# Optimization experiments

Hardware: AMD Instinct MI355X
Metric: run time of the kernel (lower is better)

## Reference

```python
import jax, jax.numpy as jnp
import numpy as np
import math

D_MODEL = 1024
N_HEADS = 16
D_K = D_MODEL // N_HEADS
THETA = 0.1


def setup_inputs() -> dict:
    key = jax.random.key(0)
    ks = jax.random.split(key, 6)
    scale = np.sqrt(1.0 / D_MODEL).astype(np.float32)
    x = jax.random.normal(ks[0], (4, 2048, D_MODEL), dtype=jnp.float32)
    W_q = jax.random.normal(ks[1], (D_MODEL, D_MODEL), dtype=jnp.float32) * scale
    W_k = jax.random.normal(ks[2], (D_MODEL, D_MODEL), dtype=jnp.float32) * scale
    W_v = jax.random.normal(ks[3], (D_MODEL, D_MODEL), dtype=jnp.float32) * scale
    W_o = jax.random.normal(ks[4], (D_MODEL, D_MODEL), dtype=jnp.float32) * scale
    alpha = jnp.ones((1,), dtype=jnp.float32)
    return {"x": x, "W_q": W_q, "W_k": W_k, "W_v": W_v, "W_o": W_o, "alpha": alpha}


def reference(x, W_q, W_k, W_v, W_o, alpha):
    B, S, _ = x.shape
    Q = x @ W_q
    K = x @ W_k
    V = x @ W_v
    # non-commutative elementwise transforms
    Q = Q + THETA * jnp.sin(Q)
    K = K + THETA * jnp.cos(K)
    V = V + alpha * THETA * jnp.tanh(V)
    # split heads: [B, H, S, d_k]
    def split(t):
        return t.reshape(B, S, N_HEADS, D_K).transpose(0, 2, 1, 3)
    Qh, Kh, Vh = split(Q), split(K), split(V)
    scores = jnp.einsum('bhqd,bhkd->bhqk', Qh, Kh) / math.sqrt(D_K)
    attn = jax.nn.softmax(scores, axis=-1)
    out = jnp.einsum('bhqk,bhkd->bhqd', attn, Vh)
    out = out.transpose(0, 2, 1, 3).reshape(B, S, D_MODEL)
    return out @ W_o
```

## Files before the change

### kernel.cpp

```cpp
#include <hip/hip_runtime.h>

typedef __bf16 bf16x8 __attribute__((ext_vector_type(8)));
typedef float f32x4 __attribute__((ext_vector_type(4)));
typedef float f32x16 __attribute__((ext_vector_type(16)));

#define MFMA16(a,b,c) __builtin_amdgcn_mfma_f32_16x16x32_bf16(a,b,c,0,0,0)
#define MFMA32(a,b,c) __builtin_amdgcn_mfma_f32_32x32x16_bf16(a,b,c,0,0,0)

__device__ __forceinline__ unsigned short f2bf(float f) {
  unsigned int u = __float_as_uint(f);
  u = (u + 0x7FFFu + ((u >> 16) & 1u)) >> 16;
  return (unsigned short)u;
}

__device__ __forceinline__ void gload16(const void* g, void* l) {
  __builtin_amdgcn_global_load_lds(
      (const __attribute__((address_space(1))) void*)g,
      (__attribute__((address_space(3))) void*)l, 16, 0, 0);
}

__device__ __forceinline__ float vexp2(float x) {
  float r;
  asm("v_exp_f32 %0, %1" : "=v"(r) : "v"(x));
  return r;
}

__device__ __forceinline__ bf16x8 mk_pfrag(int hi, float p0, float p1, float p2, float p3,
                                           float p4, float p5, float p6, float p7) {
  unsigned int a0, a1, b0, b1;
  asm("v_cvt_pk_bf16_f32 %0, %1, %2" : "=v"(a0) : "v"(p0), "v"(p1));
  asm("v_cvt_pk_bf16_f32 %0, %1, %2" : "=v"(a1) : "v"(p2), "v"(p3));
  asm("v_cvt_pk_bf16_f32 %0, %1, %2" : "=v"(b0) : "v"(p4), "v"(p5));
  asm("v_cvt_pk_bf16_f32 %0, %1, %2" : "=v"(b1) : "v"(p6), "v"(p7));
  unsigned int x = __shfl_xor(hi ? a0 : b0, 32);
  unsigned int y = __shfl_xor(hi ? a1 : b1, 32);
  uint4 w;
  w.x = hi ? x : a0;
  w.y = hi ? y : a1;
  w.z = hi ? b0 : x;
  w.w = hi ? b1 : y;
  return *reinterpret_cast<bf16x8*>(&w);
}

__global__ __launch_bounds__(256) void k_convx(const float* __restrict__ x,
                                               unsigned short* __restrict__ xb) {
  int i = (blockIdx.x * 256 + threadIdx.x) * 4;
  float4 v = *reinterpret_cast<const float4*>(x + i);
  ushort4 o;
  o.x = f2bf(v.x); o.y = f2bf(v.y); o.z = f2bf(v.z); o.w = f2bf(v.w);
  *reinterpret_cast<ushort4*>(xb + i) = o;
}

__global__ __launch_bounds__(256) void k_transw(const float* __restrict__ W,
                                                unsigned short* __restrict__ WT) {
  __shared__ float t[32][33];
  int bx = blockIdx.x * 32;
  int by = blockIdx.y * 32;
  int tx = threadIdx.x & 31;
  int ty = threadIdx.x >> 5;
#pragma unroll
  for (int i = 0; i < 32; i += 8)
    t[ty + i][tx] = W[(size_t)(by + ty + i) * 1024 + bx + tx];
  __syncthreads();
#pragma unroll
  for (int i = 0; i < 32; i += 8)
    WT[(size_t)(bx + ty + i) * 1024 + by + tx] = f2bf(t[tx][ty + i]);
}

template <int EPI>
__global__ __launch_bounds__(256) void k_gemm(
    const unsigned short* __restrict__ A, const unsigned short* __restrict__ BT, int K,
    unsigned short* __restrict__ Qf, unsigned short* __restrict__ Kf,
    unsigned short* __restrict__ VT, const float* __restrict__ alphaPtr,
    float* __restrict__ Out) {
  __shared__ __align__(16) unsigned short smem[128 * 136];
  unsigned short* As = smem;
  unsigned short* Bs = smem + 8192;
  const int tid = threadIdx.x;
  const int wave = tid >> 6, lane = tid & 63;
  const int l15 = lane & 15, lg = lane >> 4;
  const int l7 = l15 & 7;
  const int wr = wave >> 1, wc = wave & 1;
  const int bm = blockIdx.x, bn = blockIdx.y;

  f32x4 acc[4][4] = {};
  const unsigned short* Ab = A + (size_t)bm * 128 * K;
  const unsigned short* Bb = BT + (size_t)bn * 128 * K;

  const int srow = wave * 8 + (lane >> 3);
  const int scol = ((lane & 7) ^ (lane >> 3)) << 3;

  for (int k0 = 0; k0 < K; k0 += 64) {
#pragma unroll
    for (int c = 0; c < 4; ++c) {
      gload16((const void*)(Ab + (size_t)(32 * c + srow) * K + k0 + scol),
              (char*)As + c * 4096 + wave * 1024);
      gload16((const void*)(Bb + (size_t)(32 * c + srow) * K + k0 + scol),
              (char*)Bs + c * 4096 + wave * 1024);
    }
    __syncthreads();
#pragma unroll
    for (int kk = 0; kk < 2; ++kk) {
      bf16x8 af[4], bfr[4];
#pragma unroll
      for (int mi = 0; mi < 4; ++mi) {
        int R = wr * 64 + mi * 16 + l15;
        af[mi] = *reinterpret_cast<const bf16x8*>(&As[R * 64 + (((kk * 4 + lg)) ^ l7) * 8]);
      }
#pragma unroll
      for (int ni = 0; ni < 4; ++ni) {
        int R = wc * 64 + ni * 16 + l15;
        bfr[ni] = *reinterpret_cast<const bf16x8*>(&Bs[R * 64 + (((kk * 4 + lg)) ^ l7) * 8]);
      }
      __builtin_amdgcn_s_setprio(1);
#pragma unroll
      for (int mi = 0; mi < 4; ++mi)
#pragma unroll
        for (int ni = 0; ni < 4; ++ni)
          acc[mi][ni] = MFMA16(af[mi], bfr[ni], acc[mi][ni]);
      __builtin_amdgcn_s_setprio(0);
    }
    __syncthreads();
  }

  if (EPI == 0) {
    const float av = alphaPtr[0];
    const int t = bn >> 3;
    if (t == 2) {
#pragma unroll
      for (int mi = 0; mi < 4; ++mi) {
        int row0 = bm * 128 + wr * 64 + mi * 16 + lg * 4;
        int bb = row0 >> 11, s = row0 & 2047;
#pragma unroll
        for (int ni = 0; ni < 4; ++ni) {
          int col = (bn & 7) * 128 + wc * 64 + ni * 16 + l15;
          int hh = col >> 6, dd = col & 63;
          ushort4 pk;
#pragma unroll
          for (int r = 0; r < 4; ++r) {
            float v = acc[mi][ni][r];
            float e = __expf(2.0f * v);
            v += av * 0.1f * (1.0f - 2.0f * __builtin_amdgcn_rcpf(e + 1.0f));
            ((unsigned short*)&pk)[r] = f2bf(v);
          }
          *reinterpret_cast<ushort4*>(VT + ((size_t)(bb * 16 + hh) * 64 + dd) * 2048 + s) = pk;
        }
      }
    } else {
#pragma unroll
      for (int mi = 0; mi < 4; ++mi)
#pragma unroll
        for (int ni = 0; ni < 4; ++ni)
#pragma unroll
          for (int r = 0; r < 4; ++r) {
            int row = wr * 64 + mi * 16 + lg * 4 + r;
            int col = wc * 64 + ni * 16 + l15;
            float v = acc[mi][ni][r];
            if (t == 0) {
              v += 0.1f * __sinf(v);
              v *= 0.18033688011112042f;
            } else {
              v += 0.1f * __cosf(v);
            }
            smem[row * 136 + col] = f2bf(v);
          }
      __syncthreads();
      unsigned short* dst = (t == 0) ? Qf : Kf;
      const int c16 = tid & 15, rb = tid >> 4;
      const int ncol0 = (bn & 7) * 128;
#pragma unroll
      for (int i2 = 0; i2 < 8; ++i2) {
        int srow2 = rb + i2 * 16;
        uint4 val = *reinterpret_cast<const uint4*>(&smem[srow2 * 136 + c16 * 8]);
        *reinterpret_cast<uint4*>(dst + (size_t)(bm * 128 + srow2) * 1024 + ncol0 + c16 * 8) = val;
      }
    }
  } else {
#pragma unroll
    for (int ni = 0; ni < 4; ++ni) {
      int n = bn * 128 + wc * 64 + ni * 16 + l15;
#pragma unroll
      for (int mi = 0; mi < 4; ++mi) {
        int row = bm * 128 + wr * 64 + mi * 16 + lg * 4;
#pragma unroll
        for (int r = 0; r < 4; ++r)
          Out[(size_t)(row + r) * 1024 + n] = acc[mi][ni][r];
      }
    }
  }
}

__global__ __launch_bounds__(256)
__attribute__((amdgpu_waves_per_eu(4, 4)))
void k_attn(const unsigned short* __restrict__ Qf,
            const unsigned short* __restrict__ Kf,
            const unsigned short* __restrict__ VT,
            unsigned short* __restrict__ AO) {
  __shared__ __align__(16) unsigned short smem[3 * 8192];
  const int tid = threadIdx.x;
  const int wave = tid >> 6, lane = tid & 63;
  const int l31 = lane & 31, hi = lane >> 5;
  const int f = (blockIdx.y << 4) | blockIdx.x;
  const int nf = ((f & 7) << 7) | (f >> 3);
  const int qb = nf & 15, bh = nf >> 4;
  const int b = bh >> 4, h = bh & 15;

  const unsigned short* Qb = Qf + ((size_t)b * 2048 + qb * 128 + wave * 32) * 1024 + h * 64;
  const unsigned short* Kb = Kf + (size_t)b * 2048 * 1024 + h * 64;
  const unsigned short* Vb = VT + (size_t)bh * 64 * 2048;

  bf16x8 qfr[4];
#pragma unroll
  for (int ds = 0; ds < 4; ++ds)
    qfr[ds] = *reinterpret_cast<const bf16x8*>(Qb + (size_t)l31 * 1024 + ds * 16 + hi * 8);
  asm volatile("s_waitcnt vmcnt(0)" ::: "memory");

  float lsum = 0.f;
  f32x16 o0 = {}, o1 = {};

  const int krow0 = wave * 16 + (lane >> 3);
  const int ksrcc = ((lane & 7) ^ (lane >> 3)) << 3;
  const int kxor = l31 & 7;

#pragma unroll
  for (int tt = 0; tt < 2; ++tt) {
    char* Kd = (char*)(smem + tt * 8192) + wave * 2048;
    char* Vd = (char*)(smem + tt * 8192 + 4096) + wave * 2048;
    int kn = tt * 64;
    gload16((const void*)(Kb + (size_t)(kn + krow0) * 1024 + ksrcc), Kd);
    gload16((const void*)(Kb + (size_t)(kn + krow0 + 8) * 1024 + ksrcc), Kd + 1024);
    gload16((const void*)(Vb + (size_t)krow0 * 2048 + kn + ksrcc), Vd);
    gload16((const void*)(Vb + (size_t)(krow0 + 8) * 2048 + kn + ksrcc), Vd + 1024);
  }

  for (int t = 0; t < 32; ++t) {
    const unsigned short* KsC = smem + (t % 3) * 8192;
    const unsigned short* VTC = KsC + 4096;

    if (t < 31) asm volatile("s_waitcnt vmcnt(4)" ::: "memory");
    else        asm volatile("s_waitcnt vmcnt(0)" ::: "memory");
    __builtin_amdgcn_s_barrier();
    __builtin_amdgcn_sched_barrier(0);

    if (t < 30) {
      int kn = (t + 2) * 64;
      char* Kd = (char*)(smem + ((t + 2) % 3) * 8192) + wave * 2048;
      char* Vd = (char*)(smem + ((t + 2) % 3) * 8192 + 4096) + wave * 2048;
      gload16((const void*)(Kb + (size_t)(kn + krow0) * 1024 + ksrcc), Kd);
      gload16((const void*)(Kb + (size_t)(kn + krow0 + 8) * 1024 + ksrcc), Kd + 1024);
      gload16((const void*)(Vb + (size_t)krow0 * 2048 + kn + ksrcc), Vd);
      gload16((const void*)(Vb + (size_t)(krow0 + 8) * 2048 + kn + ksrcc), Vd + 1024);
    }

    f32x16 s0 = {}, s1 = {};
    __builtin_amdgcn_s_setprio(1);
#pragma unroll
    for (int ds = 0; ds < 4; ++ds) {
      int ch = ((ds * 2 + hi) ^ kxor) * 8;
      bf16x8 kf0 = *reinterpret_cast<const bf16x8*>(&KsC[l31 * 64 + ch]);
      bf16x8 kf1 = *reinterpret_cast<const bf16x8*>(&KsC[(l31 + 32) * 64 + ch]);
      s0 = MFMA32(kf0, qfr[ds], s0);
      s1 = MFMA32(kf1, qfr[ds], s1);
    }
    __builtin_amdgcn_s_setprio(0);

    float rs0 = 0.f, rs1 = 0.f, rs2 = 0.f, rs3 = 0.f;
#pragma unroll
    for (int r = 0; r < 16; r += 4) {
      float p0 = vexp2(s0[r]);     s0[r] = p0;     rs0 += p0;
      float p1 = vexp2(s0[r + 1]); s0[r + 1] = p1; rs1 += p1;
      float p2 = vexp2(s0[r + 2]); s0[r + 2] = p2; rs2 += p2;
      float p3 = vexp2(s0[r + 3]); s0[r + 3] = p3; rs3 += p3;
    }
#pragma unroll
    for (int r = 0; r < 16; r += 4) {
      float p0 = vexp2(s1[r]);     s1[r] = p0;     rs0 += p0;
      float p1 = vexp2(s1[r + 1]); s1[r + 1] = p1; rs1 += p1;
      float p2 = vexp2(s1[r + 2]); s1[r + 2] = p2; rs2 += p2;
      float p3 = vexp2(s1[r + 3]); s1[r + 3] = p3; rs3 += p3;
    }
    lsum += (rs0 + rs1) + (rs2 + rs3);

    __builtin_amdgcn_s_setprio(1);
#pragma unroll
    for (int ks = 0; ks < 4; ++ks) {
      bf16x8 pf =
          (ks == 0) ? mk_pfrag(hi, s0[0], s0[1], s0[2], s0[3], s0[4], s0[5], s0[6], s0[7])
        : (ks == 1) ? mk_pfrag(hi, s0[8], s0[9], s0[10], s0[11], s0[12], s0[13], s0[14], s0[15])
        : (ks == 2) ? mk_pfrag(hi, s1[0], s1[1], s1[2], s1[3], s1[4], s1[5], s1[6], s1[7])
                    : mk_pfrag(hi, s1[8], s1[9], s1[10], s1[11], s1[12], s1[13], s1[14], s1[15]);
      int ch = ((ks * 2 + hi) ^ kxor) * 8;
      bf16x8 v0 = *reinterpret_cast<const bf16x8*>(&VTC[l31 * 64 + ch]);
      bf16x8 v1 = *reinterpret_cast<const bf16x8*>(&VTC[(l31 + 32) * 64 + ch]);
      o0 = MFMA32(v0, pf, o0);
      o1 = MFMA32(v1, pf, o1);
    }
    __builtin_amdgcn_s_setprio(0);
  }
  __syncthreads();

  lsum += __shfl_xor(lsum, 32);
  const float inv = 1.0f / lsum;
  unsigned short* OL = smem + wave * 2304;
#pragma unroll
  for (int r = 0; r < 16; ++r) {
    int d0 = (r & 3) + 8 * (r >> 2) + 4 * hi;
    OL[l31 * 72 + d0] = f2bf(o0[r] * inv);
    OL[l31 * 72 + 32 + d0] = f2bf(o1[r] * inv);
  }
  __syncthreads();
#pragma unroll
  for (int p = 0; p < 4; ++p) {
    int u = tid + p * 256;
    int row = u >> 3, ch = u & 7;
    uint4 val = *reinterpret_cast<const uint4*>(&smem[(row >> 5) * 2304 + (row & 31) * 72 + ch * 8]);
    *reinterpret_cast<uint4*>(AO + ((size_t)b * 2048 + qb * 128 + row) * 1024 + h * 64 + ch * 8) = val;
  }
}

extern "C" void kernel_launch(void* const* d_in, const int* in_sizes, int n_in,
                              void* d_out, int out_size, void* d_ws, size_t ws_size,
                              hipStream_t stream) {
  const float* x = (const float*)d_in[0];
  const float* Wq = (const float*)d_in[1];
  const float* Wk = (const float*)d_in[2];
  const float* Wv = (const float*)d_in[3];
  const float* Wo = (const float*)d_in[4];
  const float* alpha = (const float*)d_in[5];
  float* out = (float*)d_out;

  char* ws = (char*)d_ws;
  unsigned short* xb  = (unsigned short*)(ws);
  unsigned short* WT3 = (unsigned short*)(ws + 16777216);
  unsigned short* WoT = (unsigned short*)(ws + 23068672);
  unsigned short* Qf  = (unsigned short*)(ws + 25165824);
  unsigned short* Kf  = (unsigned short*)(ws + 41943040);
  unsigned short* VTb = (unsigned short*)(ws + 58720256);
  unsigned short* AO  = (unsigned short*)(ws + 75497472);

  k_convx<<<dim3(8192), dim3(256), 0, stream>>>(x, xb);
  k_transw<<<dim3(32, 32), dim3(256), 0, stream>>>(Wq, WT3);
  k_transw<<<dim3(32, 32), dim3(256), 0, stream>>>(Wk, WT3 + 1024 * 1024);
  k_transw<<<dim3(32, 32), dim3(256), 0, stream>>>(Wv, WT3 + 2 * 1024 * 1024);
  k_transw<<<dim3(32, 32), dim3(256), 0, stream>>>(Wo, WoT);

  k_gemm<0><<<dim3(64, 24), dim3(256), 0, stream>>>(xb, WT3, 1024, Qf, Kf, VTb, alpha, nullptr);
  k_attn<<<dim3(16, 64), dim3(256), 0, stream>>>(Qf, Kf, VTb, AO);
  k_gemm<1><<<dim3(64, 8), dim3(256), 0, stream>>>(AO, WoT, 1024, nullptr, nullptr, nullptr, nullptr, out);
}
```

Before: 219.4 us.

## Process two 128-row query tiles per attention block to reuse K/V tiles

```diff
diff --git a/kernel.cpp b/kernel.cpp
--- a/kernel.cpp
+++ b/kernel.cpp
@@ -191,7 +191,6 @@
 }
 
 __global__ __launch_bounds__(256)
-__attribute__((amdgpu_waves_per_eu(4, 4)))
 void k_attn(const unsigned short* __restrict__ Qf,
             const unsigned short* __restrict__ Kf,
             const unsigned short* __restrict__ VT,
@@ -200,23 +199,26 @@
   const int tid = threadIdx.x;
   const int wave = tid >> 6, lane = tid & 63;
   const int l31 = lane & 31, hi = lane >> 5;
-  const int f = (blockIdx.y << 4) | blockIdx.x;
-  const int nf = ((f & 7) << 7) | (f >> 3);
-  const int qb = nf & 15, bh = nf >> 4;
+  const int f = (blockIdx.y << 3) | blockIdx.x;
+  const int nf = ((f & 7) << 6) | (f >> 3);
+  const int qb = nf & 7, bh = nf >> 3;
   const int b = bh >> 4, h = bh & 15;
 
-  const unsigned short* Qb = Qf + ((size_t)b * 2048 + qb * 128 + wave * 32) * 1024 + h * 64;
+  const unsigned short* QbA = Qf + ((size_t)b * 2048 + qb * 256 + wave * 32) * 1024 + h * 64;
+  const unsigned short* QbB = QbA + (size_t)128 * 1024;
   const unsigned short* Kb = Kf + (size_t)b * 2048 * 1024 + h * 64;
   const unsigned short* Vb = VT + (size_t)bh * 64 * 2048;
 
-  bf16x8 qfr[4];
-#pragma unroll
-  for (int ds = 0; ds < 4; ++ds)
-    qfr[ds] = *reinterpret_cast<const bf16x8*>(Qb + (size_t)l31 * 1024 + ds * 16 + hi * 8);
+  bf16x8 qfrA[4], qfrB[4];
+#pragma unroll
+  for (int ds = 0; ds < 4; ++ds) {
+    qfrA[ds] = *reinterpret_cast<const bf16x8*>(QbA + (size_t)l31 * 1024 + ds * 16 + hi * 8);
+    qfrB[ds] = *reinterpret_cast<const bf16x8*>(QbB + (size_t)l31 * 1024 + ds * 16 + hi * 8);
+  }
   asm volatile("s_waitcnt vmcnt(0)" ::: "memory");
 
-  float lsum = 0.f;
-  f32x16 o0 = {}, o1 = {};
+  float lsumA = 0.f, lsumB = 0.f;
+  f32x16 o0a = {}, o1a = {}, o0b = {}, o1b = {};
 
   const int krow0 = wave * 16 + (lane >> 3);
   const int ksrcc = ((lane & 7) ^ (lane >> 3)) << 3;
@@ -252,61 +254,93 @@
       gload16((const void*)(Vb + (size_t)(krow0 + 8) * 2048 + kn + ksrcc), Vd + 1024);
     }
 
-    f32x16 s0 = {}, s1 = {};
+    f32x16 s0a = {}, s1a = {}, s0b = {}, s1b = {};
     __builtin_amdgcn_s_setprio(1);
 #pragma unroll
     for (int ds = 0; ds < 4; ++ds) {
       int ch = ((ds * 2 + hi) ^ kxor) * 8;
       bf16x8 kf0 = *reinterpret_cast<const bf16x8*>(&KsC[l31 * 64 + ch]);
       bf16x8 kf1 = *reinterpret_cast<const bf16x8*>(&KsC[(l31 + 32) * 64 + ch]);
-      s0 = MFMA32(kf0, qfr[ds], s0);
-      s1 = MFMA32(kf1, qfr[ds], s1);
+      s0a = MFMA32(kf0, qfrA[ds], s0a);
+      s1a = MFMA32(kf1, qfrA[ds], s1a);
+      s0b = MFMA32(kf0, qfrB[ds], s0b);
+      s1b = MFMA32(kf1, qfrB[ds], s1b);
     }
     __builtin_amdgcn_s_setprio(0);
 
-    float rs0 = 0.f, rs1 = 0.f, rs2 = 0.f, rs3 = 0.f;
-#pragma unroll
-    for (int r = 0; r < 16; r += 4) {
-      float p0 = vexp2(s0[r]);     s0[r] = p0;     rs0 += p0;
-      float p1 = vexp2(s0[r + 1]); s0[r + 1] = p1; rs1 += p1;
-      float p2 = vexp2(s0[r + 2]); s0[r + 2] = p2; rs2 += p2;
-      float p3 = vexp2(s0[r + 3]); s0[r + 3] = p3; rs3 += p3;
-    }
-#pragma unroll
-    for (int r = 0; r < 16; r += 4) {
-      float p0 = vexp2(s1[r]);     s1[r] = p0;     rs0 += p0;
-      float p1 = vexp2(s1[r + 1]); s1[r + 1] = p1; rs1 += p1;
-      float p2 = vexp2(s1[r + 2]); s1[r + 2] = p2; rs2 += p2;
-      float p3 = vexp2(s1[r + 3]); s1[r + 3] = p3; rs3 += p3;
-    }
-    lsum += (rs0 + rs1) + (rs2 + rs3);
+    {
+      float rs0 = 0.f, rs1 = 0.f, rs2 = 0.f, rs3 = 0.f;
+#pragma unroll
+      for (int r = 0; r < 16; r += 4) {
+        float p0 = vexp2(s0a[r]);     s0a[r] = p0;     rs0 += p0;
+        float p1 = vexp2(s0a[r + 1]); s0a[r + 1] = p1; rs1 += p1;
+        float p2 = vexp2(s0a[r + 2]); s0a[r + 2] = p2; rs2 += p2;
+        float p3 = vexp2(s0a[r + 3]); s0a[r + 3] = p3; rs3 += p3;
+      }
+#pragma unroll
+      for (int r = 0; r < 16; r += 4) {
+        float p0 = vexp2(s1a[r]);     s1a[r] = p0;     rs0 += p0;
+        float p1 = vexp2(s1a[r + 1]); s1a[r + 1] = p1; rs1 += p1;
+        float p2 = vexp2(s1a[r + 2]); s1a[r + 2] = p2; rs2 += p2;
+        float p3 = vexp2(s1a[r + 3]); s1a[r + 3] = p3; rs3 += p3;
+      }
+      lsumA += (rs0 + rs1) + (rs2 + rs3);
+    }
+    {
+      float rs0 = 0.f, rs1 = 0.f, rs2 = 0.f, rs3 = 0.f;
+#pragma unroll
+      for (int r = 0; r < 16; r += 4) {
+        float p0 = vexp2(s0b[r]);     s0b[r] = p0;     rs0 += p0;
+        float p1 = vexp2(s0b[r + 1]); s0b[r + 1] = p1; rs1 += p1;
+        float p2 = vexp2(s0b[r + 2]); s0b[r + 2] = p2; rs2 += p2;
+        float p3 = vexp2(s0b[r + 3]); s0b[r + 3] = p3; rs3 += p3;
+      }
+#pragma unroll
+      for (int r = 0; r < 16; r += 4) {
+        float p0 = vexp2(s1b[r]);     s1b[r] = p0;     rs0 += p0;
+        float p1 = vexp2(s1b[r + 1]); s1b[r + 1] = p1; rs1 += p1;
+        float p2 = vexp2(s1b[r + 2]); s1b[r + 2] = p2; rs2 += p2;
+        float p3 = vexp2(s1b[r + 3]); s1b[r + 3] = p3; rs3 += p3;
+      }
+      lsumB += (rs0 + rs1) + (rs2 + rs3);
+    }
 
     __builtin_amdgcn_s_setprio(1);
 #pragma unroll
     for (int ks = 0; ks < 4; ++ks) {
-      bf16x8 pf =
-          (ks == 0) ? mk_pfrag(hi, s0[0], s0[1], s0[2], s0[3], s0[4], s0[5], s0[6], s0[7])
-        : (ks == 1) ? mk_pfrag(hi, s0[8], s0[9], s0[10], s0[11], s0[12], s0[13], s0[14], s0[15])
-        : (ks == 2) ? mk_pfrag(hi, s1[0], s1[1], s1[2], s1[3], s1[4], s1[5], s1[6], s1[7])
-                    : mk_pfrag(hi, s1[8], s1[9], s1[10], s1[11], s1[12], s1[13], s1[14], s1[15]);
+      bf16x8 pfA =
+          (ks == 0) ? mk_pfrag(hi, s0a[0], s0a[1], s0a[2], s0a[3], s0a[4], s0a[5], s0a[6], s0a[7])
+        : (ks == 1) ? mk_pfrag(hi, s0a[8], s0a[9], s0a[10], s0a[11], s0a[12], s0a[13], s0a[14], s0a[15])
+        : (ks == 2) ? mk_pfrag(hi, s1a[0], s1a[1], s1a[2], s1a[3], s1a[4], s1a[5], s1a[6], s1a[7])
+                    : mk_pfrag(hi, s1a[8], s1a[9], s1a[10], s1a[11], s1a[12], s1a[13], s1a[14], s1a[15]);
+      bf16x8 pfB =
+          (ks == 0) ? mk_pfrag(hi, s0b[0], s0b[1], s0b[2], s0b[3], s0b[4], s0b[5], s0b[6], s0b[7])
+        : (ks == 1) ? mk_pfrag(hi, s0b[8], s0b[9], s0b[10], s0b[11], s0b[12], s0b[13], s0b[14], s0b[15])
+        : (ks == 2) ? mk_pfrag(hi, s1b[0], s1b[1], s1b[2], s1b[3], s1b[4], s1b[5], s1b[6], s1b[7])
+                    : mk_pfrag(hi, s1b[8], s1b[9], s1b[10], s1b[11], s1b[12], s1b[13], s1b[14], s1b[15]);
       int ch = ((ks * 2 + hi) ^ kxor) * 8;
       bf16x8 v0 = *reinterpret_cast<const bf16x8*>(&VTC[l31 * 64 + ch]);
       bf16x8 v1 = *reinterpret_cast<const bf16x8*>(&VTC[(l31 + 32) * 64 + ch]);
-      o0 = MFMA32(v0, pf, o0);
-      o1 = MFMA32(v1, pf, o1);
+      o0a = MFMA32(v0, pfA, o0a);
+      o1a = MFMA32(v1, pfA, o1a);
+      o0b = MFMA32(v0, pfB, o0b);
+      o1b = MFMA32(v1, pfB, o1b);
     }
     __builtin_amdgcn_s_setprio(0);
   }
   __syncthreads();
 
-  lsum += __shfl_xor(lsum, 32);
-  const float inv = 1.0f / lsum;
+  lsumA += __shfl_xor(lsumA, 32);
+  lsumB += __shfl_xor(lsumB, 32);
+  const float invA = 1.0f / lsumA;
+  const float invB = 1.0f / lsumB;
   unsigned short* OL = smem + wave * 2304;
+
 #pragma unroll
   for (int r = 0; r < 16; ++r) {
     int d0 = (r & 3) + 8 * (r >> 2) + 4 * hi;
-    OL[l31 * 72 + d0] = f2bf(o0[r] * inv);
-    OL[l31 * 72 + 32 + d0] = f2bf(o1[r] * inv);
+    OL[l31 * 72 + d0] = f2bf(o0a[r] * invA);
+    OL[l31 * 72 + 32 + d0] = f2bf(o1a[r] * invA);
   }
   __syncthreads();
 #pragma unroll
@@ -314,7 +348,23 @@
     int u = tid + p * 256;
     int row = u >> 3, ch = u & 7;
     uint4 val = *reinterpret_cast<const uint4*>(&smem[(row >> 5) * 2304 + (row & 31) * 72 + ch * 8]);
-    *reinterpret_cast<uint4*>(AO + ((size_t)b * 2048 + qb * 128 + row) * 1024 + h * 64 + ch * 8) = val;
+    *reinterpret_cast<uint4*>(AO + ((size_t)b * 2048 + qb * 256 + row) * 1024 + h * 64 + ch * 8) = val;
+  }
+  __syncthreads();
+
+#pragma unroll
+  for (int r = 0; r < 16; ++r) {
+    int d0 = (r & 3) + 8 * (r >> 2) + 4 * hi;
+    OL[l31 * 72 + d0] = f2bf(o0b[r] * invB);
+    OL[l31 * 72 + 32 + d0] = f2bf(o1b[r] * invB);
+  }
+  __syncthreads();
+#pragma unroll
+  for (int p = 0; p < 4; ++p) {
+    int u = tid + p * 256;
+    int row = u >> 3, ch = u & 7;
+    uint4 val = *reinterpret_cast<const uint4*>(&smem[(row >> 5) * 2304 + (row & 31) * 72 + ch * 8]);
+    *reinterpret_cast<uint4*>(AO + ((size_t)b * 2048 + qb * 256 + 128 + row) * 1024 + h * 64 + ch * 8) = val;
   }
 }
 
@@ -345,6 +395,6 @@
   k_transw<<<dim3(32, 32), dim3(256), 0, stream>>>(Wo, WoT);
 
   k_gemm<0><<<dim3(64, 24), dim3(256), 0, stream>>>(xb, WT3, 1024, Qf, Kf, VTb, alpha, nullptr);
-  k_attn<<<dim3(16, 64), dim3(256), 0, stream>>>(Qf, Kf, VTb, AO);
+  k_attn<<<dim3(8, 64), dim3(256), 0, stream>>>(Qf, Kf, VTb, AO);
   k_gemm<1><<<dim3(64, 8), dim3(256), 0, stream>>>(AO, WoT, 1024, nullptr, nullptr, nullptr, nullptr, out);
 }
```

Measured after the change: 229.6 us. 4.7% more time.

## Load K fragments directly from global, double-buffer only V in LDS

Applied to the files above, without the earlier changes.

```diff
diff --git a/kernel.cpp b/kernel.cpp
--- a/kernel.cpp
+++ b/kernel.cpp
@@ -191,12 +191,11 @@
 }
 
 __global__ __launch_bounds__(256)
-__attribute__((amdgpu_waves_per_eu(4, 4)))
 void k_attn(const unsigned short* __restrict__ Qf,
             const unsigned short* __restrict__ Kf,
             const unsigned short* __restrict__ VT,
             unsigned short* __restrict__ AO) {
-  __shared__ __align__(16) unsigned short smem[3 * 8192];
+  __shared__ __align__(16) unsigned short smem[9216];
   const int tid = threadIdx.x;
   const int wave = tid >> 6, lane = tid & 63;
   const int l31 = lane & 31, hi = lane >> 5;
@@ -213,7 +212,6 @@
 #pragma unroll
   for (int ds = 0; ds < 4; ++ds)
     qfr[ds] = *reinterpret_cast<const bf16x8*>(Qb + (size_t)l31 * 1024 + ds * 16 + hi * 8);
-  asm volatile("s_waitcnt vmcnt(0)" ::: "memory");
 
   float lsum = 0.f;
   f32x16 o0 = {}, o1 = {};
@@ -222,32 +220,20 @@
   const int ksrcc = ((lane & 7) ^ (lane >> 3)) << 3;
   const int kxor = l31 & 7;
 
-#pragma unroll
-  for (int tt = 0; tt < 2; ++tt) {
-    char* Kd = (char*)(smem + tt * 8192) + wave * 2048;
-    char* Vd = (char*)(smem + tt * 8192 + 4096) + wave * 2048;
-    int kn = tt * 64;
-    gload16((const void*)(Kb + (size_t)(kn + krow0) * 1024 + ksrcc), Kd);
-    gload16((const void*)(Kb + (size_t)(kn + krow0 + 8) * 1024 + ksrcc), Kd + 1024);
-    gload16((const void*)(Vb + (size_t)krow0 * 2048 + kn + ksrcc), Vd);
-    gload16((const void*)(Vb + (size_t)(krow0 + 8) * 2048 + kn + ksrcc), Vd + 1024);
-  }
+  {
+    char* Vd = (char*)smem + wave * 2048;
+    gload16((const void*)(Vb + (size_t)krow0 * 2048 + ksrcc), Vd);
+    gload16((const void*)(Vb + (size_t)(krow0 + 8) * 2048 + ksrcc), Vd + 1024);
+  }
+  __syncthreads();
 
   for (int t = 0; t < 32; ++t) {
-    const unsigned short* KsC = smem + (t % 3) * 8192;
-    const unsigned short* VTC = KsC + 4096;
-
-    if (t < 31) asm volatile("s_waitcnt vmcnt(4)" ::: "memory");
-    else        asm volatile("s_waitcnt vmcnt(0)" ::: "memory");
-    __builtin_amdgcn_s_barrier();
-    __builtin_amdgcn_sched_barrier(0);
-
-    if (t < 30) {
-      int kn = (t + 2) * 64;
-      char* Kd = (char*)(smem + ((t + 2) % 3) * 8192) + wave * 2048;
-      char* Vd = (char*)(smem + ((t + 2) % 3) * 8192 + 4096) + wave * 2048;
-      gload16((const void*)(Kb + (size_t)(kn + krow0) * 1024 + ksrcc), Kd);
-      gload16((const void*)(Kb + (size_t)(kn + krow0 + 8) * 1024 + ksrcc), Kd + 1024);
+    const unsigned short* VTC = smem + (t & 1) * 4096;
+    const unsigned short* Kp = Kb + (size_t)t * 64 * 1024;
+
+    if (t < 31) {
+      int kn = (t + 1) * 64;
+      char* Vd = (char*)(smem + ((t + 1) & 1) * 4096) + wave * 2048;
       gload16((const void*)(Vb + (size_t)krow0 * 2048 + kn + ksrcc), Vd);
       gload16((const void*)(Vb + (size_t)(krow0 + 8) * 2048 + kn + ksrcc), Vd + 1024);
     }
@@ -256,9 +242,8 @@
     __builtin_amdgcn_s_setprio(1);
 #pragma unroll
     for (int ds = 0; ds < 4; ++ds) {
-      int ch = ((ds * 2 + hi) ^ kxor) * 8;
-      bf16x8 kf0 = *reinterpret_cast<const bf16x8*>(&KsC[l31 * 64 + ch]);
-      bf16x8 kf1 = *reinterpret_cast<const bf16x8*>(&KsC[(l31 + 32) * 64 + ch]);
+      bf16x8 kf0 = *reinterpret_cast<const bf16x8*>(Kp + (size_t)l31 * 1024 + ds * 16 + hi * 8);
+      bf16x8 kf1 = *reinterpret_cast<const bf16x8*>(Kp + (size_t)(l31 + 32) * 1024 + ds * 16 + hi * 8);
       s0 = MFMA32(kf0, qfr[ds], s0);
       s1 = MFMA32(kf1, qfr[ds], s1);
     }
@@ -296,8 +281,8 @@
       o1 = MFMA32(v1, pf, o1);
     }
     __builtin_amdgcn_s_setprio(0);
-  }
-  __syncthreads();
+    __syncthreads();
+  }
 
   lsum += __shfl_xor(lsum, 32);
   const float inv = 1.0f / lsum;
```

Result: slower. 283.8 us (+29.4%).
